# Optimization experiments

Hardware: AMD Instinct MI355X
Metric: run time of the kernel (lower is better)

The kernel has to match this reference:

```python
import jax, jax.numpy as jnp
import numpy as np

D_MODEL = 2048
NUM_HEADS = 16
HEAD_DIM = 128


def setup_inputs() -> dict:
    key = jax.random.key(0)
    ks = jax.random.split(key, 9)
    B, S = 2, 2048
    s_in = 1.0 / np.sqrt(D_MODEL)
    return {
        "x": jax.random.normal(ks[0], (B, S, D_MODEL), dtype=jnp.float32),
        "wq": jax.random.normal(ks[1], (D_MODEL, D_MODEL), dtype=jnp.float32) * s_in,
        "bq": jnp.zeros((D_MODEL,), jnp.float32),
        "wk": jax.random.normal(ks[2], (D_MODEL, HEAD_DIM), dtype=jnp.float32) * s_in,
        "bk": jnp.zeros((HEAD_DIM,), jnp.float32),
        "wv": jax.random.normal(ks[3], (D_MODEL, HEAD_DIM), dtype=jnp.float32) * s_in,
        "bv": jnpp_zeros(ks) if False else jnp.zeros((HEAD_DIM,), jnp.float32),
        "wo": jax.random.normal(ks[4], (D_MODEL, D_MODEL), dtype=jnp.float32) * s_in,
        "bo": jnp.zeros((D_MODEL,), jnp.float32),
    }


def reference(x, wq, bq, wk, bk, wv, bv, wo, bo):
    B, S, _ = x.shape
    H, Dh = NUM_HEADS, HEAD_DIM
    q = (x @ wq + bq).reshape(B, S, H, Dh)          # [B,S,H,Dh]
    k = x @ wk + bk                                  # [B,S,Dh] (single KV head)
    v = x @ wv + bv                                  # [B,S,Dh]
    scale = 1.0 / jnp.sqrt(jnp.asarray(Dh, x.dtype))
    # scores: [B,H,Sq,Sk] — MQA: K shared across heads
    scores = jnp.einsum('bqhd,bkd->bhqk', q, k) * scale
    attn = jax.nn.softmax(scores, axis=-1)
    out = jnp.einsum('bhqk,bkd->bqhd', attn, v).reshape(B, S, H * Dh)
    return out @ wo + bo
```

## Files before the change

kernel.cpp:

```cpp
#include <hip/hip_runtime.h>
#include <stdint.h>

typedef unsigned short u16;

#define D_MODEL 2048
#define HEADS 16
#define HDIM 128
#define SEQ 2048
#define BATCH 2
#define NROWS (BATCH*SEQ)
#define QKV_N (D_MODEL + 2*HDIM)

typedef __attribute__((ext_vector_type(8))) short bf16x8;
typedef __attribute__((ext_vector_type(4))) float f32x4;

__device__ inline u16 f2bf(float f) {
  union { float f; uint32_t u; } v; v.f = f;
  uint32_t r = v.u + 0x7FFFu + ((v.u >> 16) & 1u);
  return (u16)(r >> 16);
}
__device__ inline u16 f2bf_fast(float f) {
  union { float f; uint32_t u; } v; v.f = f;
  return (u16)((v.u + 0x8000u) >> 16);
}

__device__ inline void gload_lds16(const void* g, void* l) {
  __builtin_amdgcn_global_load_lds(
      (const __attribute__((address_space(1))) unsigned int*)g,
      (__attribute__((address_space(3))) unsigned int*)l, 16, 0, 0);
}

__global__ void prep_all(const float* __restrict__ x, u16* __restrict__ xb,
                         const float* __restrict__ wq, const float* __restrict__ wk,
                         const float* __restrict__ wv, const float* __restrict__ wo,
                         u16* __restrict__ wqkvT, u16* __restrict__ woT,
                         const float* __restrict__ bq, const float* __restrict__ bk,
                         const float* __restrict__ bv, float* __restrict__ biasq) {
  const int bid = blockIdx.x, tid = threadIdx.x;
  if (bid < 1024) {
    const float4* xf = (const float4*)x;
    ushort4* xo = (ushort4*)xb;
    int i = bid * 256 + tid;
#pragma unroll
    for (int r = 0; r < 8; r++, i += 262144) {
      float4 f = xf[i];
      ushort4 u;
      u.x = f2bf(f.x); u.y = f2bf(f.y); u.z = f2bf(f.z); u.w = f2bf(f.w);
      xo[i] = u;
    }
  } else if (bid < 9728) {
    __shared__ float t[32][33];
    const int b2 = bid - 1024;
    const int n0v = (b2 % 136) * 32, k0 = (b2 / 136) * 32;
    const float* src; int N, n0, drow; u16* dst;
    if (n0v < 2048)      { src = wq; N = 2048; n0 = n0v;        dst = wqkvT; drow = n0v; }
    else if (n0v < 2176) { src = wk; N = 128;  n0 = n0v - 2048; dst = wqkvT; drow = n0v; }
    else if (n0v < 2304) { src = wv; N = 128;  n0 = n0v - 2176; dst = wqkvT; drow = n0v; }
    else                 { src = wo; N = 2048; n0 = n0v - 2304; dst = woT;   drow = n0v - 2304; }
    const int tx = tid & 31, ty = tid >> 5;
#pragma unroll
    for (int i = 0; i < 4; i++)
      t[ty + 8*i][tx] = src[(size_t)(k0 + ty + 8*i) * N + n0 + tx];
    __syncthreads();
#pragma unroll
    for (int i = 0; i < 4; i++)
      dst[(size_t)(drow + ty + 8*i) * D_MODEL + k0 + tx] = f2bf(t[tx][ty + 8*i]);
  } else {
    for (int i = tid; i < QKV_N; i += 256)
      biasq[i] = (i < D_MODEL) ? bq[i]
               : ((i < D_MODEL + HDIM) ? bk[i - D_MODEL] : bv[i - D_MODEL - HDIM]);
  }
}

#define BM 128
#define BN 128
#define BKK 64

template <bool DB>
__global__ __launch_bounds__(256) void gemm_bt(
    const u16* __restrict__ A, const u16* __restrict__ BT,
    const float* __restrict__ bias,
    u16* __restrict__ Cb, float* __restrict__ Cf,
    u16* __restrict__ vT,
    int M, int N, int tilesN, int K) {
  __shared__ __align__(16) u16 sA[DB ? 2 : 1][BM * BKK];
  __shared__ __align__(16) u16 sB[DB ? 2 : 1][BN * BKK];
  const int tid = threadIdx.x;
  const int wave = tid >> 6, lane = tid & 63;
  const int bm = blockIdx.x / tilesN, bn = blockIdx.x % tilesN;
  const int m0 = bm * BM, n0 = bn * BN;
  const int wm = (wave & 1) * 64, wn = (wave >> 1) * 64;
  const int l16 = lane & 15, quad = lane >> 4;

  f32x4 acc[4][4] = {};

  const int dRow = lane >> 3;
  const int dCol = ((lane & 7) ^ (lane >> 3)) * 8;

#define GDMA(i, buf)                                                           \
  {                                                                            \
    const int _k0 = (i) * BKK;                                                 \
    _Pragma("unroll") for (int c = 0; c < 4; c++) {                            \
      const int op = wave * 4 + c;                                             \
      const int row = op * 8 + dRow;                                           \
      gload_lds16(&A[(size_t)(m0 + row) * K + _k0 + dCol], &sA[buf][op * 512]);\
      gload_lds16(&BT[(size_t)(n0 + row) * K + _k0 + dCol], &sB[buf][op * 512]);\
    }                                                                          \
  }

  const int NI = K / BKK;
  GDMA(0, 0);
  for (int i = 0; i < NI; i++) {
    const int cur = DB ? (i & 1) : 0;
    __syncthreads();
    if (DB && i + 1 < NI) GDMA(i + 1, cur ^ 1);
#pragma unroll
    for (int kk2 = 0; kk2 < 2; kk2++) {
      bf16x8 af[4], bfr[4];
#pragma unroll
      for (int mb = 0; mb < 4; ++mb) {
        const int R = wm + mb * 16 + l16;
        const int s = (kk2 * 4 + quad) ^ (l16 & 7);
        af[mb] = *(const bf16x8*)&sA[cur][R * BKK + s * 8];
      }
#pragma unroll
      for (int nb = 0; nb < 4; ++nb) {
        const int R = wn + nb * 16 + l16;
        const int s = (kk2 * 4 + quad) ^ (l16 & 7);
        bfr[nb] = *(const bf16x8*)&sB[cur][R * BKK + s * 8];
      }
#pragma unroll
      for (int mb = 0; mb < 4; ++mb)
#pragma unroll
        for (int nb = 0; nb < 4; ++nb)
          acc[mb][nb] = __builtin_amdgcn_mfma_f32_16x16x32_bf16(af[mb], bfr[nb], acc[mb][nb], 0, 0, 0);
    }
    if (!DB) {
      __syncthreads();
      if (i + 1 < NI) GDMA(i + 1, 0);
    }
  }
#undef GDMA

#pragma unroll
  for (int mb = 0; mb < 4; ++mb) {
#pragma unroll
    for (int nb = 0; nb < 4; ++nb) {
      const int gn = n0 + wn + nb * 16 + l16;
      const float bb = bias ? bias[gn] : 0.0f;
#pragma unroll
      for (int r = 0; r < 4; ++r) {
        const int gm = m0 + wm + mb * 16 + quad * 4 + r;
        const float v = acc[mb][nb][r] + bb;
        if (Cf) {
          Cf[(size_t)gm * N + gn] = v;
        } else {
          const u16 u = f2bf(v);
          Cb[(size_t)gm * N + gn] = u;
          if (vT && gn >= D_MODEL + HDIM) {
            const int bi = gm >> 11, si = gm & 2047;
            vT[((size_t)bi * HDIM + (gn - D_MODEL - HDIM)) * SEQ + si] = u;
          }
        }
      }
    }
  }
}

__global__ __launch_bounds__(256) void mqa_attn(
    const u16* __restrict__ qkv, const u16* __restrict__ vT, u16* __restrict__ ctx) {
  __shared__ __align__(16) u16 sK[2][64 * 128];
  __shared__ __align__(16) u16 sV[128 * 64];
  __shared__ __align__(16) u16 sP[4][32 * 64];
  const int tid = threadIdx.x, wave = tid >> 6, lane = tid & 63;
  const int qt = blockIdx.x & 15;
  const int h  = (blockIdx.x >> 4) & 15;
  const int b  = blockIdx.x >> 8;
  const int bS = b * SEQ;
  const int q0 = qt * 128 + wave * 32;
  const int l16 = lane & 15, quad = lane >> 4;
  const int sw = l16 & 7;
  u16* myP = &sP[wave][0];

  bf16x8 qf[2][4];
#pragma unroll
  for (int mb = 0; mb < 2; mb++)
#pragma unroll
    for (int kc = 0; kc < 4; kc++)
      qf[mb][kc] = *(const bf16x8*)&qkv[(size_t)(bS + q0 + mb*16 + l16) * QKV_N
                                        + h*HDIM + kc*32 + quad*8];

  f32x4 o[2][8] = {};
  float lrow[2] = {0.f, 0.f};
  const float sc2 = 0.08838834764831845f * 1.4426950408889634f;

  const u16* Kbase = qkv + (size_t)bS * QKV_N + D_MODEL;
  const u16* Vbase = vT + (size_t)b * HDIM * SEQ;

  const int kRowIn = lane >> 4;
  const int kChS   = lane & 15;
  const int vRowIn = lane >> 3;
  const int vChL   = (lane & 7) ^ (lane >> 3);

#define DMA_K(t, dst)                                                          \
  {                                                                            \
    const int _sk = (t) * 64;                                                  \
    _Pragma("unroll") for (int j = 0; j < 4; j++) {                            \
      const int i = wave * 4 + j;                                              \
      const int krow = i * 4 + kRowIn;                                         \
      const int kcl = kChS ^ (krow & 15);                                      \
      gload_lds16(&Kbase[(size_t)(_sk + krow) * QKV_N + kcl * 8],              \
                  &(dst)[i * 512]);                                            \
    }                                                                          \
  }
#define DMA_V(t)                                                               \
  {                                                                            \
    const int _sk = (t) * 64;                                                  \
    _Pragma("unroll") for (int j = 0; j < 4; j++) {                            \
      const int i = wave * 4 + j;                                              \
      const int d = i * 8 + vRowIn;                                            \
      gload_lds16(&Vbase[(size_t)d * SEQ + _sk + vChL * 8], &sV[i * 512]);     \
    }                                                                          \
  }

  DMA_K(0, sK[0]);
  DMA_V(0);
  __syncthreads();

  const int T = SEQ / 64;
  for (int t = 0; t < T; ++t) {
    const int cur = t & 1;
    if (t + 1 < T) DMA_K(t + 1, sK[cur ^ 1]);

    f32x4 sc[2][4];
    __builtin_amdgcn_s_setprio(1);
#pragma unroll
    for (int nb = 0; nb < 4; nb++) {
      bf16x8 kf[4];
#pragma unroll
      for (int kc = 0; kc < 4; kc++)
        kf[kc] = *(const bf16x8*)&sK[cur][(nb*16 + l16) * 128 + (((kc*4 + quad) ^ l16) * 8)];
#pragma unroll
      for (int mb = 0; mb < 2; mb++) {
        f32x4 a = {0.f, 0.f, 0.f, 0.f};
#pragma unroll
        for (int kc = 0; kc < 4; kc++)
          a = __builtin_amdgcn_mfma_f32_16x16x32_bf16(kf[kc], qf[mb][kc], a, 0, 0, 0);
        sc[mb][nb] = a;
      }
    }
    __builtin_amdgcn_s_setprio(0);

#pragma unroll
    for (int mb = 0; mb < 2; mb++)
#pragma unroll
      for (int nb = 0; nb < 4; nb++) {
        float p0 = __builtin_amdgcn_exp2f(sc[mb][nb][0] * sc2);
        float p1 = __builtin_amdgcn_exp2f(sc[mb][nb][1] * sc2);
        float p2 = __builtin_amdgcn_exp2f(sc[mb][nb][2] * sc2);
        float p3 = __builtin_amdgcn_exp2f(sc[mb][nb][3] * sc2);
        lrow[mb] += (p0 + p1) + (p2 + p3);
        uint32_t lo = (uint32_t)f2bf_fast(p0) | ((uint32_t)f2bf_fast(p1) << 16);
        uint32_t hi = (uint32_t)f2bf_fast(p2) | ((uint32_t)f2bf_fast(p3) << 16);
        uint2 w; w.x = lo; w.y = hi;
        const int pr = (nb*2 + (quad >> 1)) ^ sw;
        *(uint2*)&myP[(mb*16 + l16) * 64 + pr * 8 + (quad & 1) * 4] = w;
      }

    __syncthreads();

    bf16x8 pf[2][2];
#pragma unroll
    for (int mb = 0; mb < 2; mb++)
#pragma unroll
      for (int kc = 0; kc < 2; kc++)
        pf[mb][kc] = *(const bf16x8*)&myP[(mb*16 + l16) * 64 + (((kc*4 + quad) ^ sw) * 8)];

    __builtin_amdgcn_s_setprio(1);
#pragma unroll
    for (int nb = 0; nb < 8; nb++) {
      bf16x8 vf[2];
#pragma unroll
      for (int kc = 0; kc < 2; kc++)
        vf[kc] = *(const bf16x8*)&sV[(nb*16 + l16) * 64 + (((kc*4 + quad) ^ (l16 & 7)) * 8)];
#pragma unroll
      for (int mb = 0; mb < 2; mb++)
#pragma unroll
        for (int kc = 0; kc < 2; kc++)
          o[mb][nb] = __builtin_amdgcn_mfma_f32_16x16x32_bf16(pf[mb][kc], vf[kc], o[mb][nb], 0, 0, 0);
    }
    __builtin_amdgcn_s_setprio(0);

    __syncthreads();
    if (t + 1 < T) DMA_V(t + 1);
  }

#pragma unroll
  for (int mb = 0; mb < 2; mb++) {
    lrow[mb] += __shfl_xor(lrow[mb], 16, 64);
    lrow[mb] += __shfl_xor(lrow[mb], 32, 64);
  }
  float invl[2][4];
#pragma unroll
  for (int mb = 0; mb < 2; mb++)
#pragma unroll
    for (int r = 0; r < 4; r++)
      invl[mb][r] = 1.0f / __shfl(lrow[mb], quad * 4 + r, 64);

#pragma unroll
  for (int mb = 0; mb < 2; mb++)
#pragma unroll
    for (int nb = 0; nb < 8; nb++)
#pragma unroll
      for (int r = 0; r < 4; r++) {
        const int gq = q0 + mb*16 + quad*4 + r;
        const int gd = h * HDIM + nb*16 + l16;
        ctx[(size_t)(bS + gq) * D_MODEL + gd] = f2bf(o[mb][nb][r] * invl[mb][r]);
      }
}

extern "C" void kernel_launch(void* const* d_in, const int* in_sizes, int n_in,
                              void* d_out, int out_size, void* d_ws, size_t ws_size,
                              hipStream_t stream) {
  const float* x  = (const float*)d_in[0];
  const float* wq = (const float*)d_in[1];
  const float* bq = (const float*)d_in[2];
  const float* wk = (const float*)d_in[3];
  const float* bk = (const float*)d_in[4];
  const float* wv = (const float*)d_in[5];
  const float* bv = (const float*)d_in[6];
  const float* wo = (const float*)d_in[7];
  const float* bo = (const float*)d_in[8];
  float* out = (float*)d_out;
  char* ws = (char*)d_ws;

  u16*   xb    = (u16*)(ws + 0);
  u16*   wqkvT = (u16*)(ws + 16777216);
  u16*   woT   = (u16*)(ws + 26214400);
  u16*   qkv   = (u16*)(ws + 34603008);
  u16*   vT    = (u16*)(ws + 53477376);
  u16*   ctx   = (u16*)(ws + 54525952);
  float* biasq = (float*)(ws + 71303168);

  prep_all<<<9729, 256, 0, stream>>>(x, xb, wq, wk, wv, wo, wqkvT, woT,
                                     bq, bk, bv, biasq);
  gemm_bt<false><<<32 * 18, 256, 0, stream>>>(xb, wqkvT, biasq, qkv, nullptr, vT,
                                              NROWS, QKV_N, 18, D_MODEL);
  mqa_attn<<<BATCH * HEADS * (SEQ / 128), 256, 0, stream>>>(qkv, vT, ctx);
  gemm_bt<true><<<32 * 16, 256, 0, stream>>>(ctx, woT, bo, nullptr, out, nullptr,
                                             NROWS, D_MODEL, 16, D_MODEL);
}
```

Measured before the change: 302.1 us.

## Fold softmax scale into Wq, drop setprio, add GEMM launch-bound occupancy hints

The softmax scale times log2(e) is now folded into the bf16 copy of Wq and into bq during prep, so the attention kernel calls exp2 on raw scores without a per-element multiply. The s_setprio hints around the MFMA loops are removed. Each GEMM instantiation also gets a minimum-waves launch bound (3 for QKV, 2 for output) to push register allocation toward higher occupancy. Scaling Q before the bf16 rounding changes rounding slightly, and the tighter launch bounds risk register spills.

```diff
diff --git a/kernel.cpp b/kernel.cpp
--- a/kernel.cpp
+++ b/kernel.cpp
@@ -10,6 +10,8 @@
 #define BATCH 2
 #define NROWS (BATCH*SEQ)
 #define QKV_N (D_MODEL + 2*HDIM)
+
+#define SC2F 0.12751743f
 
 typedef __attribute__((ext_vector_type(8))) short bf16x8;
 typedef __attribute__((ext_vector_type(4))) float f32x4;
@@ -52,8 +54,8 @@
     __shared__ float t[32][33];
     const int b2 = bid - 1024;
     const int n0v = (b2 % 136) * 32, k0 = (b2 / 136) * 32;
-    const float* src; int N, n0, drow; u16* dst;
-    if (n0v < 2048)      { src = wq; N = 2048; n0 = n0v;        dst = wqkvT; drow = n0v; }
+    const float* src; int N, n0, drow; u16* dst; float scl = 1.0f;
+    if (n0v < 2048)      { src = wq; N = 2048; n0 = n0v;        dst = wqkvT; drow = n0v; scl = SC2F; }
     else if (n0v < 2176) { src = wk; N = 128;  n0 = n0v - 2048; dst = wqkvT; drow = n0v; }
     else if (n0v < 2304) { src = wv; N = 128;  n0 = n0v - 2176; dst = wqkvT; drow = n0v; }
     else                 { src = wo; N = 2048; n0 = n0v - 2304; dst = woT;   drow = n0v - 2304; }
@@ -64,10 +66,10 @@
     __syncthreads();
 #pragma unroll
     for (int i = 0; i < 4; i++)
-      dst[(size_t)(drow + ty + 8*i) * D_MODEL + k0 + tx] = f2bf(t[tx][ty + 8*i]);
+      dst[(size_t)(drow + ty + 8*i) * D_MODEL + k0 + tx] = f2bf(t[tx][ty + 8*i] * scl);
   } else {
     for (int i = tid; i < QKV_N; i += 256)
-      biasq[i] = (i < D_MODEL) ? bq[i]
+      biasq[i] = (i < D_MODEL) ? bq[i] * SC2F
                : ((i < D_MODEL + HDIM) ? bk[i - D_MODEL] : bv[i - D_MODEL - HDIM]);
   }
 }
@@ -76,8 +78,8 @@
 #define BN 128
 #define BKK 64
 
-template <bool DB>
-__global__ __launch_bounds__(256) void gemm_bt(
+template <bool DB, int MINW>
+__global__ __launch_bounds__(256, MINW) void gemm_bt(
     const u16* __restrict__ A, const u16* __restrict__ BT,
     const float* __restrict__ bias,
     u16* __restrict__ Cb, float* __restrict__ Cf,
@@ -192,7 +194,6 @@
 
   f32x4 o[2][8] = {};
   float lrow[2] = {0.f, 0.f};
-  const float sc2 = 0.08838834764831845f * 1.4426950408889634f;
 
   const u16* Kbase = qkv + (size_t)bS * QKV_N + D_MODEL;
   const u16* Vbase = vT + (size_t)b * HDIM * SEQ;
@@ -233,7 +234,6 @@
     if (t + 1 < T) DMA_K(t + 1, sK[cur ^ 1]);
 
     f32x4 sc[2][4];
-    __builtin_amdgcn_s_setprio(1);
 #pragma unroll
     for (int nb = 0; nb < 4; nb++) {
       bf16x8 kf[4];
@@ -249,16 +249,15 @@
         sc[mb][nb] = a;
       }
     }
-    __builtin_amdgcn_s_setprio(0);
 
 #pragma unroll
     for (int mb = 0; mb < 2; mb++)
 #pragma unroll
       for (int nb = 0; nb < 4; nb++) {
-        float p0 = __builtin_amdgcn_exp2f(sc[mb][nb][0] * sc2);
-        float p1 = __builtin_amdgcn_exp2f(sc[mb][nb][1] * sc2);
-        float p2 = __builtin_amdgcn_exp2f(sc[mb][nb][2] * sc2);
-        float p3 = __builtin_amdgcn_exp2f(sc[mb][nb][3] * sc2);
+        float p0 = __builtin_amdgcn_exp2f(sc[mb][nb][0]);
+        float p1 = __builtin_amdgcn_exp2f(sc[mb][nb][1]);
+        float p2 = __builtin_amdgcn_exp2f(sc[mb][nb][2]);
+        float p3 = __builtin_amdgcn_exp2f(sc[mb][nb][3]);
         lrow[mb] += (p0 + p1) + (p2 + p3);
         uint32_t lo = (uint32_t)f2bf_fast(p0) | ((uint32_t)f2bf_fast(p1) << 16);
         uint32_t hi = (uint32_t)f2bf_fast(p2) | ((uint32_t)f2bf_fast(p3) << 16);
@@ -276,7 +275,6 @@
       for (int kc = 0; kc < 2; kc++)
         pf[mb][kc] = *(const bf16x8*)&myP[(mb*16 + l16) * 64 + (((kc*4 + quad) ^ sw) * 8)];
 
-    __builtin_amdgcn_s_setprio(1);
 #pragma unroll
     for (int nb = 0; nb < 8; nb++) {
       bf16x8 vf[2];
@@ -289,7 +287,6 @@
         for (int kc = 0; kc < 2; kc++)
           o[mb][nb] = __builtin_amdgcn_mfma_f32_16x16x32_bf16(pf[mb][kc], vf[kc], o[mb][nb], 0, 0, 0);
     }
-    __builtin_amdgcn_s_setprio(0);
 
     __syncthreads();
     if (t + 1 < T) DMA_V(t + 1);
@@ -344,9 +341,9 @@
 
   prep_all<<<9729, 256, 0, stream>>>(x, xb, wq, wk, wv, wo, wqkvT, woT,
                                      bq, bk, bv, biasq);
-  gemm_bt<false><<<32 * 18, 256, 0, stream>>>(xb, wqkvT, biasq, qkv, nullptr, vT,
-                                              NROWS, QKV_N, 18, D_MODEL);
+  gemm_bt<false, 3><<<32 * 18, 256, 0, stream>>>(xb, wqkvT, biasq, qkv, nullptr, vT,
+                                                 NROWS, QKV_N, 18, D_MODEL);
   mqa_attn<<<BATCH * HEADS * (SEQ / 128), 256, 0, stream>>>(qkv, vT, ctx);
-  gemm_bt<true><<<32 * 16, 256, 0, stream>>>(ctx, woT, bo, nullptr, out, nullptr,
-                                             NROWS, D_MODEL, 16, D_MODEL);
-}
+  gemm_bt<true, 2><<<32 * 16, 256, 0, stream>>>(ctx, woT, bo, nullptr, out, nullptr,
+                                                NROWS, D_MODEL, 16, D_MODEL);
+}
```

Result: faster. 292.6 us (-3.1%).
